# Optimization experiments

Hardware: AMD Instinct MI355X
Metric: run time of the kernel (lower is better)

The kernel has to match this reference:

```python
import jax, jax.numpy as jnp
import numpy as np
from jax import lax

NEG = -1000.0  # torch.full((N,S), -1000.0) init in dp_align


def setup_inputs() -> dict:
    key = jax.random.key(0)
    ks = jax.random.split(key, 4)
    N, S, h = 128, 2048, 256          # nodes, segments, hsize
    d = 2 * h                         # bi-LSTM output dim = 2*hsize
    seg_text_feats = jax.random.normal(ks[0], (N, d), jnp.float32)
    vid_feature = jax.random.normal(ks[1], (S, d), jnp.float32)
    # relation_query: Linear(4h, h) -> ReLU -> (Dropout, eval=identity) -> Linear(h, 1)
    W1 = jax.random.normal(ks[2], (h, 2 * d), jnp.float32) / np.sqrt(2.0 * d)
    b1 = jnp.zeros((h,), jnp.float32)
    W2 = jax.random.normal(ks[3], (1, h), jnp.float32) / np.sqrt(float(h))
    b2 = jnp.zeros((1,), jnp.float32)
    return {"seg_text_feats": seg_text_feats, "vid_feature": vid_feature,
            "W1": W1, "b1": b1, "W2": W2, "b2": b2}


def reference(seg_text_feats, vid_feature, W1, b1, W2, b2):
    N, d = seg_text_feats.shape
    S = vid_feature.shape[0]
    # Pairwise MLP logits for every (node, segment) cell, vectorized:
    # concat(text, vid) @ W1^T == text @ W1[:, :d]^T + vid @ W1[:, d:]^T
    A = seg_text_feats @ W1[:, :d].T           # [N, h]
    B = vid_feature @ W1[:, d:].T              # [S, h]
    H = jax.nn.relu(A[:, None, :] + B[None, :, :] + b1)   # [N, S, h]
    logits = jnp.einsum('nsh,h->ns', H, W2[0]) + b2[0]     # [N, S]
    logsig = jax.nn.log_sigmoid(logits)

    n_idx = jnp.arange(N)
    # DP over columns, right to left. prev_col is arr[:, s+1] (virtual col S = NEG).
    def step(prev_col, s):
        ls = logsig[:, s]
        nxt = jnp.concatenate([prev_col[1:], jnp.full((1,), NEG, prev_col.dtype)])  # arr[n+1, s+1]
        curr = ls + jnp.where(n_idx == N - 1, 0.0, nxt)   # last node: no chain term
        take = curr >= prev_col                            # tie -> take current (matches >=)
        val = jnp.where(take, curr, prev_col)
        in_range = (s >= n_idx) & (s <= S - N + n_idx)     # start_ind/end_ind bands
        col = jnp.where(in_range, val, NEG)
        return col, take

    _, takes = lax.scan(step, jnp.full((N,), NEG), jnp.arange(S - 1, -1, -1))
    take_curr = takes[::-1].T                              # [N, S]

    # Backtrack parent pointers from (node 0, segment 0).
    def walk(carry, s):
        n, align = carry
        nc = jnp.minimum(n, N - 1)
        tc = take_curr[nc, s] & (n < N)
        align = align.at[nc].set(jnp.where(tc, s, align[nc]))
        return (n + tc.astype(jnp.int32), align), None

    (_, align), _ = lax.scan(walk, (jnp.int32(0), jnp.zeros((N,), jnp.int32)), jnp.arange(S))

    aggregated_logits = jnp.mean(logits[n_idx, align])     # sum(logit)/num_nodes
    adj_matrix = jnp.zeros((N + S, N + S), jnp.float32).at[S + n_idx, align].set(1.0)
    return adj_matrix, aggregated_logits
```

## Files before the change

kernel.cpp:

```cpp
#include <hip/hip_runtime.h>
#include <math.h>

#define NEGC (-1000.0f)

__global__ __launch_bounds__(256) void k1z_gemm(
    const float* __restrict__ seg, const float* __restrict__ vid,
    const float* __restrict__ W1, const float* __restrict__ b1,
    float* __restrict__ A2, float* __restrict__ B2, float4* __restrict__ out4)
{
    if (blockIdx.x >= 136) {
        const int i = (blockIdx.x - 136) * 256 + threadIdx.x;
        if (i < 1183744) out4[i] = make_float4(0.f, 0.f, 0.f, 0.f);
        return;
    }
    __shared__ float Xs[32][64];
    __shared__ float Ws[32][64];
    const int tid = threadIdx.x;
    const int tx = tid & 15, ty = tid >> 4;
    const int lr = tid >> 2;
    const int lk = (tid & 3) * 8;
    const int colBase = (blockIdx.x & 3) * 64;
    const int rowBase = (blockIdx.x >> 2) * 64;
    const bool isSeg = (rowBase < 128);
    const float* __restrict__ X = isSeg ? seg : vid;
    const int xRow = isSeg ? rowBase : (rowBase - 128);
    const int wOff = isSeg ? 0 : 512;

    float acc[4][4] = {};

    for (int k0 = 0; k0 < 512; k0 += 32) {
        const float* xp = X + (size_t)(xRow + lr) * 512 + (k0 + lk);
        const float4 xa = *(const float4*)xp;
        const float4 xb = *(const float4*)(xp + 4);
        const float* wp = W1 + (size_t)(colBase + lr) * 1024 + (wOff + k0 + lk);
        const float4 wa = *(const float4*)wp;
        const float4 wb = *(const float4*)(wp + 4);
        __syncthreads();
        Xs[lk + 0][lr] = xa.x; Xs[lk + 1][lr] = xa.y;
        Xs[lk + 2][lr] = xa.z; Xs[lk + 3][lr] = xa.w;
        Xs[lk + 4][lr] = xb.x; Xs[lk + 5][lr] = xb.y;
        Xs[lk + 6][lr] = xb.z; Xs[lk + 7][lr] = xb.w;
        Ws[lk + 0][lr] = wa.x; Ws[lk + 1][lr] = wa.y;
        Ws[lk + 2][lr] = wa.z; Ws[lk + 3][lr] = wa.w;
        Ws[lk + 4][lr] = wb.x; Ws[lk + 5][lr] = wb.y;
        Ws[lk + 6][lr] = wb.z; Ws[lk + 7][lr] = wb.w;
        __syncthreads();
        #pragma unroll
        for (int kk = 0; kk < 32; ++kk) {
            const float4 a4 = *(const float4*)&Xs[kk][4 * ty];
            const float4 b4 = *(const float4*)&Ws[kk][4 * tx];
            const float* a = (const float*)&a4;
            const float* b = (const float*)&b4;
            #pragma unroll
            for (int i = 0; i < 4; ++i)
                #pragma unroll
                for (int j = 0; j < 4; ++j)
                    acc[i][j] = fmaf(a[i], b[j], acc[i][j]);
        }
    }

    float* __restrict__ outp = (isSeg ? A2 : B2) + (size_t)xRow * 256;
    const int c = colBase + 4 * tx;
    #pragma unroll
    for (int i = 0; i < 4; ++i) {
        float4 v = make_float4(acc[i][0], acc[i][1], acc[i][2], acc[i][3]);
        if (isSeg) {
            v.x += b1[c + 0]; v.y += b1[c + 1]; v.z += b1[c + 2]; v.w += b1[c + 3];
        }
        *(float4*)(outp + (size_t)(4 * ty + i) * 256 + c) = v;
    }
}

__global__ __launch_bounds__(256) void k2_logits(
    const float* __restrict__ A2, const float* __restrict__ B2,
    const float* __restrict__ W2, const float* __restrict__ b2p,
    float* __restrict__ logitsT, float* __restrict__ lsPK)
{
    __shared__ float As[32][64];
    __shared__ float Bs[32][64];
    __shared__ float w2s[256];
    const int tid = threadIdx.x;
    const int tx = tid & 15, ty = tid >> 4;
    const int lr = tid >> 2;
    const int lk = (tid & 3) * 8;
    const int nBase = blockIdx.x * 64;
    const int sBase = blockIdx.y * 64;
    w2s[tid] = W2[tid];
    const float b2v = b2p[0];

    float acc[4][4] = {};

    for (int k0 = 0; k0 < 256; k0 += 32) {
        const float* ap = A2 + (size_t)(nBase + lr) * 256 + (k0 + lk);
        const float4 aa = *(const float4*)ap;
        const float4 ab = *(const float4*)(ap + 4);
        const float* bp = B2 + (size_t)(sBase + lr) * 256 + (k0 + lk);
        const float4 ba = *(const float4*)bp;
        const float4 bb = *(const float4*)(bp + 4);
        __syncthreads();
        As[lk + 0][lr] = aa.x; As[lk + 1][lr] = aa.y;
        As[lk + 2][lr] = aa.z; As[lk + 3][lr] = aa.w;
        As[lk + 4][lr] = ab.x; As[lk + 5][lr] = ab.y;
        As[lk + 6][lr] = ab.z; As[lk + 7][lr] = ab.w;
        Bs[lk + 0][lr] = ba.x; Bs[lk + 1][lr] = ba.y;
        Bs[lk + 2][lr] = ba.z; Bs[lk + 3][lr] = ba.w;
        Bs[lk + 4][lr] = bb.x; Bs[lk + 5][lr] = bb.y;
        Bs[lk + 6][lr] = bb.z; Bs[lk + 7][lr] = bb.w;
        __syncthreads();
        #pragma unroll
        for (int kk = 0; kk < 32; ++kk) {
            const float w = w2s[k0 + kk];
            const float4 a4 = *(const float4*)&As[kk][4 * ty];
            const float4 b4 = *(const float4*)&Bs[kk][4 * tx];
            const float* a = (const float*)&a4;
            const float* b = (const float*)&b4;
            #pragma unroll
            for (int i = 0; i < 4; ++i)
                #pragma unroll
                for (int j = 0; j < 4; ++j)
                    acc[i][j] = fmaf(fmaxf(a[i] + b[j], 0.0f), w, acc[i][j]);
        }
    }

    const int nb = nBase + 4 * ty;
    const int s0 = sBase + 4 * tx;
    float lsv[4][4];
    #pragma unroll
    for (int j = 0; j < 4; ++j) {
        const int s = s0 + j;
        float4 lg;
        float* lgp = (float*)&lg;
        #pragma unroll
        for (int i = 0; i < 4; ++i) {
            const float x = acc[i][j] + b2v;
            lgp[i] = x;
            lsv[j][i] = fminf(x, 0.0f) - log1pf(expf(-fabsf(x)));
        }
        *(float4*)&logitsT[(size_t)s * 128 + nb] = lg;
    }
    #pragma unroll
    for (int m = 0; m < 2; ++m) {
        const size_t base = (size_t)(s0 / 2 + m) * 256 + 2 * nb;
        #pragma unroll
        for (int q = 0; q < 2; ++q) {
            float4 v = make_float4(lsv[2 * m][2 * q],     lsv[2 * m + 1][2 * q],
                                   lsv[2 * m][2 * q + 1], lsv[2 * m + 1][2 * q + 1]);
            *(float4*)&lsPK[base + 4 * q] = v;
        }
    }
}

__global__ __launch_bounds__(64, 1) void k3_dp(
    const float* __restrict__ lsPK, const float* __restrict__ logitsT,
    float* __restrict__ out)
{
    __shared__ unsigned takeW[128 * 65];
    __shared__ int alignSh[128];
    const int lane = threadIdx.x;
    const int n0 = 2 * lane, n1 = n0 + 1;
    const float4* __restrict__ ls4 = (const float4*)lsPK;

    float p0 = NEGC, p1 = NEGC;
    unsigned u0 = 2047u - (unsigned)n0;
    unsigned u1 = u0 - 1u;
    unsigned w0 = 0u, w1 = 0u;

    auto core = [&](float lx, float ly, float nx) {
        float c0, c1;
        unsigned long long cc;
        asm volatile(
            "v_add_f32 %[c0], %[lx], %[p1]\n\t"
            "v_add_f32 %[c1], %[ly], %[nx]\n\t"
            "v_cmp_ge_f32 vcc, %[c0], %[p0]\n\t"
            "v_cmp_ge_f32 %[cc], %[c1], %[p1]\n\t"
            "v_addc_co_u32 %[w0], vcc, %[w0], %[w0], vcc\n\t"
            "v_addc_co_u32 %[w1], %[cc], %[w1], %[w1], %[cc]\n\t"
            "v_max_f32 %[p0], %[c0], %[p0]\n\t"
            "v_max_f32 %[p1], %[c1], %[p1]\n\t"
            : [p0]"+v"(p0), [p1]"+v"(p1), [w0]"+v"(w0), [w1]"+v"(w1),
              [c0]"=&v"(c0), [c1]"=&v"(c1), [cc]"=&s"(cc)
            : [lx]"v"(lx), [ly]"v"(ly), [nx]"v"(nx)
            : "vcc");
    };

    auto stepF = [&](float lx, float ly) {
        float nxt1 = __int_as_float(__builtin_amdgcn_update_dpp(
            0, __float_as_int(p0), 0x130 , 0xf, 0xf, true));
        core(lx, ly, nxt1);
    };
    auto stepM = [&](float lx, float ly) {
        float nxt1 = __int_as_float(__builtin_amdgcn_update_dpp(
            0, __float_as_int(p0), 0x130, 0xf, 0xf, true));
        core(lx, ly, nxt1);
        p0 = (u0 <= 1920u) ? p0 : NEGC;
        p1 = (u1 <= 1920u) ? p1 : NEGC;
        --u0; --u1;
    };

    float4 B0[4], B1[4], B2[4], B3[4], B4[4], B5[4], B6[4], B7[4];
#define LOADG(B, H) { _Pragma("unroll") \
    for (int j = 0; j < 4; ++j) B[j] = ls4[(size_t)((1023 - 4 * (H) - j) * 64 + lane)]; }
#define STEPS_F(B) { _Pragma("unroll") \
    for (int j = 0; j < 4; ++j) { stepF(B[j].y, B[j].w); stepF(B[j].x, B[j].z); } }
#define STEPS_M(B) { _Pragma("unroll") \
    for (int j = 0; j < 4; ++j) { stepM(B[j].y, B[j].w); stepM(B[j].x, B[j].z); } }
#define FLUSH { takeW[n0 * 65 + wIdx] = w0; takeW[n1 * 65 + wIdx] = w1; \
                w0 = 0u; w1 = 0u; --wIdx; }
#define BODY(SM) \
    SM(B0); if (h +  8 < 256) LOADG(B0, h +  8); \
    SM(B1); if (h +  9 < 256) LOADG(B1, h +  9); \
    SM(B2); if (h + 10 < 256) LOADG(B2, h + 10); \
    SM(B3); FLUSH; if (h + 11 < 256) LOADG(B3, h + 11); \
    SM(B4); if (h + 12 < 256) LOADG(B4, h + 12); \
    SM(B5); if (h + 13 < 256) LOADG(B5, h + 13); \
    SM(B6); if (h + 14 < 256) LOADG(B6, h + 14); \
    SM(B7); FLUSH; if (h + 15 < 256) LOADG(B7, h + 15);

    LOADG(B0, 0) LOADG(B1, 1) LOADG(B2, 2) LOADG(B3, 3)
    LOADG(B4, 4) LOADG(B5, 5) LOADG(B6, 6) LOADG(B7, 7)
    int wIdx = 63;
    for (int h = 0; h < 16; h += 8) { BODY(STEPS_M) }
    for (int h = 16; h < 240; h += 8) { BODY(STEPS_F) }
    u0 = (unsigned)(127 - n0);
    u1 = u0 - 1u;
    for (int h = 240; h < 256; h += 8) { BODY(STEPS_M) }
#undef BODY
#undef FLUSH
#undef STEPS_M
#undef STEPS_F
#undef LOADG

    alignSh[n0] = 0;
    alignSh[n1] = 0;
    __syncthreads();

    int pos = 0;
    for (int n = 0; n < 128; ++n) {
        unsigned w = takeW[n * 65 + lane];
        const int wi0 = pos >> 5;
        if (lane < wi0) w = 0u;
        else if (lane == wi0) w &= (0xFFFFFFFFu << (pos & 31));
        const unsigned long long m = __ballot(w != 0u);
        if (m == 0ull) break;
        const int fl = __builtin_ctzll(m);
        const unsigned fw = (unsigned)__builtin_amdgcn_readlane((int)w, fl);
        const int s = fl * 32 + __builtin_ctz(fw);
        if (lane == 0) alignSh[n] = s;
        pos = s + 1;
    }
    __syncthreads();

    const int a0 = alignSh[n0];
    const int a1 = alignSh[n1];
    out[(size_t)(2048 + n0) * 2176 + a0] = 1.0f;
    out[(size_t)(2048 + n1) * 2176 + a1] = 1.0f;
    float sum = logitsT[(size_t)a0 * 128 + n0] + logitsT[(size_t)a1 * 128 + n1];
    #pragma unroll
    for (int off = 32; off >= 1; off >>= 1) sum += __shfl_down(sum, off);
    if (lane == 0) out[(size_t)2176 * 2176] = sum * (1.0f / 128.0f);
}

extern "C" void kernel_launch(void* const* d_in, const int* in_sizes, int n_in,
                              void* d_out, int out_size, void* d_ws, size_t ws_size,
                              hipStream_t stream)
{
    const float* seg = (const float*)d_in[0];
    const float* vid = (const float*)d_in[1];
    const float* W1  = (const float*)d_in[2];
    const float* b1  = (const float*)d_in[3];
    const float* W2  = (const float*)d_in[4];
    const float* b2  = (const float*)d_in[5];
    float* out = (float*)d_out;
    float* ws  = (float*)d_ws;

    float* A2      = ws;
    float* B2      = ws + 32768;
    float* logitsT = ws + 557056;
    float* lsPK    = ws + 819200;

    k1z_gemm<<<dim3(4760), dim3(256), 0, stream>>>(seg, vid, W1, b1, A2, B2, (float4*)out);
    k2_logits<<<dim3(2, 32), dim3(256), 0, stream>>>(A2, B2, W2, b2, logitsT, lsPK);
    k3_dp<<<dim3(1), dim3(64), 0, stream>>>(lsPK, logitsT, out);
}
```

Measured before the change: 193.7 us.

## Use producer waves to stage DP inputs through double-buffered LDS ring

The serial DP kernel grows from one wave to four. Three producer waves prefetch log-sigmoid columns from global memory into a double-buffered shared-memory ring, while wave 0 consumes windows of 32 float4 columns from LDS. The aim is to take global-load latency off the single-wave critical path. In exchange it adds a block-wide barrier per window and LDS read latency on the consumer, and the backtrack now keeps alignments in registers instead of shared memory.

```diff
diff --git a/kernel.cpp b/kernel.cpp
--- a/kernel.cpp
+++ b/kernel.cpp
@@ -150,15 +150,33 @@
     }
 }
 
-__global__ __launch_bounds__(64, 1) void k3_dp(
+__global__ __launch_bounds__(256, 1) void k3_dp(
     const float* __restrict__ lsPK, const float* __restrict__ logitsT,
     float* __restrict__ out)
 {
+    __shared__ float4 ring[2][2048];
     __shared__ unsigned takeW[128 * 65];
-    __shared__ int alignSh[128];
-    const int lane = threadIdx.x;
+    const int tid = threadIdx.x;
+    const int wave = tid >> 6;
+    const int lane = tid & 63;
     const int n0 = 2 * lane, n1 = n0 + 1;
     const float4* __restrict__ ls4 = (const float4*)lsPK;
+
+    auto produce = [&](int k) {
+        const size_t base = (size_t)(992 - 32 * k) * 64 + lane;
+        const int p = wave - 1;
+        float4 t[11];
+        #pragma unroll
+        for (int i = 0; i < 11; ++i) {
+            const int c = p + 3 * i;
+            if (c < 32) t[i] = ls4[base + (size_t)c * 64];
+        }
+        #pragma unroll
+        for (int i = 0; i < 11; ++i) {
+            const int c = p + 3 * i;
+            if (c < 32) ring[k & 1][c * 64 + lane] = t[i];
+        }
+    };
 
     float p0 = NEGC, p1 = NEGC;
     unsigned u0 = 2047u - (unsigned)n0;
@@ -197,44 +215,52 @@
         --u0; --u1;
     };
 
-    float4 B0[4], B1[4], B2[4], B3[4], B4[4], B5[4], B6[4], B7[4];
-#define LOADG(B, H) { _Pragma("unroll") \
-    for (int j = 0; j < 4; ++j) B[j] = ls4[(size_t)((1023 - 4 * (H) - j) * 64 + lane)]; }
-#define STEPS_F(B) { _Pragma("unroll") \
-    for (int j = 0; j < 4; ++j) { stepF(B[j].y, B[j].w); stepF(B[j].x, B[j].z); } }
-#define STEPS_M(B) { _Pragma("unroll") \
-    for (int j = 0; j < 4; ++j) { stepM(B[j].y, B[j].w); stepM(B[j].x, B[j].z); } }
+    float4 C0, C1, C2, C3, N0, N1, N2, N3;
+    int wIdx = 63;
+#define RD(B, OFF) B = rb[(OFF) * 64 + lane];
+#define CONS4(STEP, Ba, Bb, Bc, Bd) { \
+    STEP(Ba.y, Ba.w); STEP(Ba.x, Ba.z); STEP(Bb.y, Bb.w); STEP(Bb.x, Bb.z); \
+    STEP(Bc.y, Bc.w); STEP(Bc.x, Bc.z); STEP(Bd.y, Bd.w); STEP(Bd.x, Bd.z); }
 #define FLUSH { takeW[n0 * 65 + wIdx] = w0; takeW[n1 * 65 + wIdx] = w1; \
                 w0 = 0u; w1 = 0u; --wIdx; }
-#define BODY(SM) \
-    SM(B0); if (h +  8 < 256) LOADG(B0, h +  8); \
-    SM(B1); if (h +  9 < 256) LOADG(B1, h +  9); \
-    SM(B2); if (h + 10 < 256) LOADG(B2, h + 10); \
-    SM(B3); FLUSH; if (h + 11 < 256) LOADG(B3, h + 11); \
-    SM(B4); if (h + 12 < 256) LOADG(B4, h + 12); \
-    SM(B5); if (h + 13 < 256) LOADG(B5, h + 13); \
-    SM(B6); if (h + 14 < 256) LOADG(B6, h + 14); \
-    SM(B7); FLUSH; if (h + 15 < 256) LOADG(B7, h + 15);
-
-    LOADG(B0, 0) LOADG(B1, 1) LOADG(B2, 2) LOADG(B3, 3)
-    LOADG(B4, 4) LOADG(B5, 5) LOADG(B6, 6) LOADG(B7, 7)
-    int wIdx = 63;
-    for (int h = 0; h < 16; h += 8) { BODY(STEPS_M) }
-    for (int h = 16; h < 240; h += 8) { BODY(STEPS_F) }
-    u0 = (unsigned)(127 - n0);
-    u1 = u0 - 1u;
-    for (int h = 240; h < 256; h += 8) { BODY(STEPS_M) }
-#undef BODY
+#define WINDOW(STEP) { \
+    RD(C0,31) RD(C1,30) RD(C2,29) RD(C3,28) \
+    RD(N0,27) RD(N1,26) RD(N2,25) RD(N3,24) CONS4(STEP,C0,C1,C2,C3) \
+    RD(C0,23) RD(C1,22) RD(C2,21) RD(C3,20) CONS4(STEP,N0,N1,N2,N3) \
+    RD(N0,19) RD(N1,18) RD(N2,17) RD(N3,16) CONS4(STEP,C0,C1,C2,C3) \
+    RD(C0,15) RD(C1,14) RD(C2,13) RD(C3,12) CONS4(STEP,N0,N1,N2,N3) FLUSH \
+    RD(N0,11) RD(N1,10) RD(N2, 9) RD(N3, 8) CONS4(STEP,C0,C1,C2,C3) \
+    RD(C0, 7) RD(C1, 6) RD(C2, 5) RD(C3, 4) CONS4(STEP,N0,N1,N2,N3) \
+    RD(N0, 3) RD(N1, 2) RD(N2, 1) RD(N3, 0) CONS4(STEP,C0,C1,C2,C3) \
+    CONS4(STEP,N0,N1,N2,N3) FLUSH }
+
+    if (wave > 0) produce(0);
+    __syncthreads();
+
+    for (int k = 0; k < 32; ++k) {
+        if (wave > 0) {
+            if (k + 1 < 32) produce(k + 1);
+        } else {
+            const float4* rb = &ring[k & 1][0];
+            if (k < 2) {
+                WINDOW(stepM)
+            } else if (k < 30) {
+                WINDOW(stepF)
+            } else {
+                if (k == 30) { u0 = (unsigned)(127 - n0); u1 = u0 - 1u; }
+                WINDOW(stepM)
+            }
+        }
+        __syncthreads();
+    }
+#undef WINDOW
 #undef FLUSH
-#undef STEPS_M
-#undef STEPS_F
-#undef LOADG
-
-    alignSh[n0] = 0;
-    alignSh[n1] = 0;
-    __syncthreads();
-
-    int pos = 0;
+#undef CONS4
+#undef RD
+
+    if (wave != 0) return;
+
+    int a0r = 0, a1r = 0, pos = 0;
     for (int n = 0; n < 128; ++n) {
         unsigned w = takeW[n * 65 + lane];
         const int wi0 = pos >> 5;
@@ -245,16 +271,14 @@
         const int fl = __builtin_ctzll(m);
         const unsigned fw = (unsigned)__builtin_amdgcn_readlane((int)w, fl);
         const int s = fl * 32 + __builtin_ctz(fw);
-        if (lane == 0) alignSh[n] = s;
+        if (n == n0) a0r = s;
+        if (n == n1) a1r = s;
         pos = s + 1;
     }
-    __syncthreads();
-
-    const int a0 = alignSh[n0];
-    const int a1 = alignSh[n1];
-    out[(size_t)(2048 + n0) * 2176 + a0] = 1.0f;
-    out[(size_t)(2048 + n1) * 2176 + a1] = 1.0f;
-    float sum = logitsT[(size_t)a0 * 128 + n0] + logitsT[(size_t)a1 * 128 + n1];
+
+    out[(size_t)(2048 + n0) * 2176 + a0r] = 1.0f;
+    out[(size_t)(2048 + n1) * 2176 + a1r] = 1.0f;
+    float sum = logitsT[(size_t)a0r * 128 + n0] + logitsT[(size_t)a1r * 128 + n1];
     #pragma unroll
     for (int off = 32; off >= 1; off >>= 1) sum += __shfl_down(sum, off);
     if (lane == 0) out[(size_t)2176 * 2176] = sum * (1.0f / 128.0f);
@@ -280,5 +304,5 @@
 
     k1z_gemm<<<dim3(4760), dim3(256), 0, stream>>>(seg, vid, W1, b1, A2, B2, (float4*)out);
     k2_logits<<<dim3(2, 32), dim3(256), 0, stream>>>(A2, B2, W2, b2, logitsT, lsPK);
-    k3_dp<<<dim3(1), dim3(64), 0, stream>>>(lsPK, logitsT, out);
+    k3_dp<<<dim3(1), dim3(256), 0, stream>>>(lsPK, logitsT, out);
 }
```

Measured after the change: 222.2 us. +14.7%, slower.

## Fuse GEMM, logits and DP kernels into one cooperative kernel with grid syncs

Applied to the files above, without the earlier changes.

Merges the three launches (projection GEMM plus output zeroing, pairwise logits, serial DP and backtrack) into a single cooperative kernel of 256 blocks separated by grid.sync barriers. Each block zeroes an equal slice of the output instead of using thousands of extra zero-fill blocks. The backtrack now keeps alignment indices in registers rather than shared memory. The aim is to remove inter-kernel launch gaps, at the cost of grid-barrier overhead, a larger shared-memory footprint per block, and heavier zeroing work per block.

```diff
diff --git a/kernel.cpp b/kernel.cpp
--- a/kernel.cpp
+++ b/kernel.cpp
@@ -1,203 +1,209 @@
 #include <hip/hip_runtime.h>
+#include <hip/hip_cooperative_groups.h>
 #include <math.h>
 
 #define NEGC (-1000.0f)
-
-__global__ __launch_bounds__(256) void k1z_gemm(
+namespace cg = cooperative_groups;
+
+__global__ __launch_bounds__(256, 1) void kfused(
     const float* __restrict__ seg, const float* __restrict__ vid,
     const float* __restrict__ W1, const float* __restrict__ b1,
-    float* __restrict__ A2, float* __restrict__ B2, float4* __restrict__ out4)
+    const float* __restrict__ W2, const float* __restrict__ b2p,
+    float* __restrict__ A2, float* __restrict__ B2,
+    float* __restrict__ logitsT, float* __restrict__ lsPK,
+    float* __restrict__ out)
 {
-    if (blockIdx.x >= 136) {
-        const int i = (blockIdx.x - 136) * 256 + threadIdx.x;
-        if (i < 1183744) out4[i] = make_float4(0.f, 0.f, 0.f, 0.f);
-        return;
-    }
     __shared__ float Xs[32][64];
     __shared__ float Ws[32][64];
+    __shared__ float w2s[256];
+    __shared__ unsigned takeW[128 * 65];
+
+    cg::grid_group grid = cg::this_grid();
+    const int bid = blockIdx.x;
     const int tid = threadIdx.x;
-    const int tx = tid & 15, ty = tid >> 4;
-    const int lr = tid >> 2;
-    const int lk = (tid & 3) * 8;
-    const int colBase = (blockIdx.x & 3) * 64;
-    const int rowBase = (blockIdx.x >> 2) * 64;
-    const bool isSeg = (rowBase < 128);
-    const float* __restrict__ X = isSeg ? seg : vid;
-    const int xRow = isSeg ? rowBase : (rowBase - 128);
-    const int wOff = isSeg ? 0 : 512;
-
-    float acc[4][4] = {};
-
-    for (int k0 = 0; k0 < 512; k0 += 32) {
-        const float* xp = X + (size_t)(xRow + lr) * 512 + (k0 + lk);
-        const float4 xa = *(const float4*)xp;
-        const float4 xb = *(const float4*)(xp + 4);
-        const float* wp = W1 + (size_t)(colBase + lr) * 1024 + (wOff + k0 + lk);
-        const float4 wa = *(const float4*)wp;
-        const float4 wb = *(const float4*)(wp + 4);
-        __syncthreads();
-        Xs[lk + 0][lr] = xa.x; Xs[lk + 1][lr] = xa.y;
-        Xs[lk + 2][lr] = xa.z; Xs[lk + 3][lr] = xa.w;
-        Xs[lk + 4][lr] = xb.x; Xs[lk + 5][lr] = xb.y;
-        Xs[lk + 6][lr] = xb.z; Xs[lk + 7][lr] = xb.w;
-        Ws[lk + 0][lr] = wa.x; Ws[lk + 1][lr] = wa.y;
-        Ws[lk + 2][lr] = wa.z; Ws[lk + 3][lr] = wa.w;
-        Ws[lk + 4][lr] = wb.x; Ws[lk + 5][lr] = wb.y;
-        Ws[lk + 6][lr] = wb.z; Ws[lk + 7][lr] = wb.w;
-        __syncthreads();
-        #pragma unroll
-        for (int kk = 0; kk < 32; ++kk) {
-            const float4 a4 = *(const float4*)&Xs[kk][4 * ty];
-            const float4 b4 = *(const float4*)&Ws[kk][4 * tx];
-            const float* a = (const float*)&a4;
-            const float* b = (const float*)&b4;
-            #pragma unroll
-            for (int i = 0; i < 4; ++i)
+
+    if (bid < 136) {
+        const int tx = tid & 15, ty = tid >> 4;
+        const int lr = tid >> 2;
+        const int lk = (tid & 3) * 8;
+        const int colBase = (bid & 3) * 64;
+        const int rowBase = (bid >> 2) * 64;
+        const bool isSeg = (rowBase < 128);
+        const float* __restrict__ X = isSeg ? seg : vid;
+        const int xRow = isSeg ? rowBase : (rowBase - 128);
+        const int wOff = isSeg ? 0 : 512;
+
+        float acc[4][4] = {};
+
+        for (int k0 = 0; k0 < 512; k0 += 32) {
+            const float* xp = X + (size_t)(xRow + lr) * 512 + (k0 + lk);
+            const float4 xa = *(const float4*)xp;
+            const float4 xb = *(const float4*)(xp + 4);
+            const float* wp = W1 + (size_t)(colBase + lr) * 1024 + (wOff + k0 + lk);
+            const float4 wa = *(const float4*)wp;
+            const float4 wb = *(const float4*)(wp + 4);
+            __syncthreads();
+            Xs[lk + 0][lr] = xa.x; Xs[lk + 1][lr] = xa.y;
+            Xs[lk + 2][lr] = xa.z; Xs[lk + 3][lr] = xa.w;
+            Xs[lk + 4][lr] = xb.x; Xs[lk + 5][lr] = xb.y;
+            Xs[lk + 6][lr] = xb.z; Xs[lk + 7][lr] = xb.w;
+            Ws[lk + 0][lr] = wa.x; Ws[lk + 1][lr] = wa.y;
+            Ws[lk + 2][lr] = wa.z; Ws[lk + 3][lr] = wa.w;
+            Ws[lk + 4][lr] = wb.x; Ws[lk + 5][lr] = wb.y;
+            Ws[lk + 6][lr] = wb.z; Ws[lk + 7][lr] = wb.w;
+            __syncthreads();
+            #pragma unroll
+            for (int kk = 0; kk < 32; ++kk) {
+                const float4 a4 = *(const float4*)&Xs[kk][4 * ty];
+                const float4 b4 = *(const float4*)&Ws[kk][4 * tx];
+                const float* a = (const float*)&a4;
+                const float* b = (const float*)&b4;
                 #pragma unroll
-                for (int j = 0; j < 4; ++j)
-                    acc[i][j] = fmaf(a[i], b[j], acc[i][j]);
-        }
-    }
-
-    float* __restrict__ outp = (isSeg ? A2 : B2) + (size_t)xRow * 256;
-    const int c = colBase + 4 * tx;
-    #pragma unroll
-    for (int i = 0; i < 4; ++i) {
-        float4 v = make_float4(acc[i][0], acc[i][1], acc[i][2], acc[i][3]);
-        if (isSeg) {
-            v.x += b1[c + 0]; v.y += b1[c + 1]; v.z += b1[c + 2]; v.w += b1[c + 3];
-        }
-        *(float4*)(outp + (size_t)(4 * ty + i) * 256 + c) = v;
-    }
-}
-
-__global__ __launch_bounds__(256) void k2_logits(
-    const float* __restrict__ A2, const float* __restrict__ B2,
-    const float* __restrict__ W2, const float* __restrict__ b2p,
-    float* __restrict__ logitsT, float* __restrict__ lsPK)
-{
-    __shared__ float As[32][64];
-    __shared__ float Bs[32][64];
-    __shared__ float w2s[256];
-    const int tid = threadIdx.x;
-    const int tx = tid & 15, ty = tid >> 4;
-    const int lr = tid >> 2;
-    const int lk = (tid & 3) * 8;
-    const int nBase = blockIdx.x * 64;
-    const int sBase = blockIdx.y * 64;
-    w2s[tid] = W2[tid];
-    const float b2v = b2p[0];
-
-    float acc[4][4] = {};
-
-    for (int k0 = 0; k0 < 256; k0 += 32) {
-        const float* ap = A2 + (size_t)(nBase + lr) * 256 + (k0 + lk);
-        const float4 aa = *(const float4*)ap;
-        const float4 ab = *(const float4*)(ap + 4);
-        const float* bp = B2 + (size_t)(sBase + lr) * 256 + (k0 + lk);
-        const float4 ba = *(const float4*)bp;
-        const float4 bb = *(const float4*)(bp + 4);
-        __syncthreads();
-        As[lk + 0][lr] = aa.x; As[lk + 1][lr] = aa.y;
-        As[lk + 2][lr] = aa.z; As[lk + 3][lr] = aa.w;
-        As[lk + 4][lr] = ab.x; As[lk + 5][lr] = ab.y;
-        As[lk + 6][lr] = ab.z; As[lk + 7][lr] = ab.w;
-        Bs[lk + 0][lr] = ba.x; Bs[lk + 1][lr] = ba.y;
-        Bs[lk + 2][lr] = ba.z; Bs[lk + 3][lr] = ba.w;
-        Bs[lk + 4][lr] = bb.x; Bs[lk + 5][lr] = bb.y;
-        Bs[lk + 6][lr] = bb.z; Bs[lk + 7][lr] = bb.w;
-        __syncthreads();
-        #pragma unroll
-        for (int kk = 0; kk < 32; ++kk) {
-            const float w = w2s[k0 + kk];
-            const float4 a4 = *(const float4*)&As[kk][4 * ty];
-            const float4 b4 = *(const float4*)&Bs[kk][4 * tx];
-            const float* a = (const float*)&a4;
-            const float* b = (const float*)&b4;
-            #pragma unroll
-            for (int i = 0; i < 4; ++i)
+                for (int i = 0; i < 4; ++i)
+                    #pragma unroll
+                    for (int j = 0; j < 4; ++j)
+                        acc[i][j] = fmaf(a[i], b[j], acc[i][j]);
+            }
+        }
+
+        float* __restrict__ outp = (isSeg ? A2 : B2) + (size_t)xRow * 256;
+        const int c = colBase + 4 * tx;
+        #pragma unroll
+        for (int i = 0; i < 4; ++i) {
+            float4 v = make_float4(acc[i][0], acc[i][1], acc[i][2], acc[i][3]);
+            if (isSeg) {
+                v.x += b1[c + 0]; v.y += b1[c + 1]; v.z += b1[c + 2]; v.w += b1[c + 3];
+            }
+            *(float4*)(outp + (size_t)(4 * ty + i) * 256 + c) = v;
+        }
+    }
+    {
+        float4* out4 = (float4*)out;
+        const int base = bid * 4624;
+        const float4 z = make_float4(0.f, 0.f, 0.f, 0.f);
+        for (int i = tid; i < 4624; i += 256) out4[base + i] = z;
+    }
+    grid.sync();
+
+    if (bid < 64) {
+        float (* __restrict__ As)[64] = Xs;
+        float (* __restrict__ Bs)[64] = Ws;
+        const int tx = tid & 15, ty = tid >> 4;
+        const int lr = tid >> 2;
+        const int lk = (tid & 3) * 8;
+        const int nBase = (bid & 1) * 64;
+        const int sBase = (bid >> 1) * 64;
+        w2s[tid] = W2[tid];
+        const float b2v = b2p[0];
+
+        float acc[4][4] = {};
+
+        for (int k0 = 0; k0 < 256; k0 += 32) {
+            const float* ap = A2 + (size_t)(nBase + lr) * 256 + (k0 + lk);
+            const float4 aa = *(const float4*)ap;
+            const float4 ab = *(const float4*)(ap + 4);
+            const float* bp = B2 + (size_t)(sBase + lr) * 256 + (k0 + lk);
+            const float4 ba = *(const float4*)bp;
+            const float4 bb = *(const float4*)(bp + 4);
+            __syncthreads();
+            As[lk + 0][lr] = aa.x; As[lk + 1][lr] = aa.y;
+            As[lk + 2][lr] = aa.z; As[lk + 3][lr] = aa.w;
+            As[lk + 4][lr] = ab.x; As[lk + 5][lr] = ab.y;
+            As[lk + 6][lr] = ab.z; As[lk + 7][lr] = ab.w;
+            Bs[lk + 0][lr] = ba.x; Bs[lk + 1][lr] = ba.y;
+            Bs[lk + 2][lr] = ba.z; Bs[lk + 3][lr] = ba.w;
+            Bs[lk + 4][lr] = bb.x; Bs[lk + 5][lr] = bb.y;
+            Bs[lk + 6][lr] = bb.z; Bs[lk + 7][lr] = bb.w;
+            __syncthreads();
+            #pragma unroll
+            for (int kk = 0; kk < 32; ++kk) {
+                const float w = w2s[k0 + kk];
+                const float4 a4 = *(const float4*)&As[kk][4 * ty];
+                const float4 b4 = *(const float4*)&Bs[kk][4 * tx];
+                const float* a = (const float*)&a4;
+                const float* b = (const float*)&b4;
                 #pragma unroll
-                for (int j = 0; j < 4; ++j)
-                    acc[i][j] = fmaf(fmaxf(a[i] + b[j], 0.0f), w, acc[i][j]);
-        }
-    }
-
-    const int nb = nBase + 4 * ty;
-    const int s0 = sBase + 4 * tx;
-    float lsv[4][4];
-    #pragma unroll
-    for (int j = 0; j < 4; ++j) {
-        const int s = s0 + j;
-        float4 lg;
-        float* lgp = (float*)&lg;
-        #pragma unroll
-        for (int i = 0; i < 4; ++i) {
-            const float x = acc[i][j] + b2v;
-            lgp[i] = x;
-            lsv[j][i] = fminf(x, 0.0f) - log1pf(expf(-fabsf(x)));
-        }
-        *(float4*)&logitsT[(size_t)s * 128 + nb] = lg;
-    }
-    #pragma unroll
-    for (int m = 0; m < 2; ++m) {
-        const size_t base = (size_t)(s0 / 2 + m) * 256 + 2 * nb;
-        #pragma unroll
-        for (int q = 0; q < 2; ++q) {
-            float4 v = make_float4(lsv[2 * m][2 * q],     lsv[2 * m + 1][2 * q],
-                                   lsv[2 * m][2 * q + 1], lsv[2 * m + 1][2 * q + 1]);
-            *(float4*)&lsPK[base + 4 * q] = v;
-        }
-    }
-}
-
-__global__ __launch_bounds__(64, 1) void k3_dp(
-    const float* __restrict__ lsPK, const float* __restrict__ logitsT,
-    float* __restrict__ out)
-{
-    __shared__ unsigned takeW[128 * 65];
-    __shared__ int alignSh[128];
-    const int lane = threadIdx.x;
-    const int n0 = 2 * lane, n1 = n0 + 1;
-    const float4* __restrict__ ls4 = (const float4*)lsPK;
-
-    float p0 = NEGC, p1 = NEGC;
-    unsigned u0 = 2047u - (unsigned)n0;
-    unsigned u1 = u0 - 1u;
-    unsigned w0 = 0u, w1 = 0u;
-
-    auto core = [&](float lx, float ly, float nx) {
-        float c0, c1;
-        unsigned long long cc;
-        asm volatile(
-            "v_add_f32 %[c0], %[lx], %[p1]\n\t"
-            "v_add_f32 %[c1], %[ly], %[nx]\n\t"
-            "v_cmp_ge_f32 vcc, %[c0], %[p0]\n\t"
-            "v_cmp_ge_f32 %[cc], %[c1], %[p1]\n\t"
-            "v_addc_co_u32 %[w0], vcc, %[w0], %[w0], vcc\n\t"
-            "v_addc_co_u32 %[w1], %[cc], %[w1], %[w1], %[cc]\n\t"
-            "v_max_f32 %[p0], %[c0], %[p0]\n\t"
-            "v_max_f32 %[p1], %[c1], %[p1]\n\t"
-            : [p0]"+v"(p0), [p1]"+v"(p1), [w0]"+v"(w0), [w1]"+v"(w1),
-              [c0]"=&v"(c0), [c1]"=&v"(c1), [cc]"=&s"(cc)
-            : [lx]"v"(lx), [ly]"v"(ly), [nx]"v"(nx)
-            : "vcc");
-    };
-
-    auto stepF = [&](float lx, float ly) {
-        float nxt1 = __int_as_float(__builtin_amdgcn_update_dpp(
-            0, __float_as_int(p0), 0x130 , 0xf, 0xf, true));
-        core(lx, ly, nxt1);
-    };
-    auto stepM = [&](float lx, float ly) {
-        float nxt1 = __int_as_float(__builtin_amdgcn_update_dpp(
-            0, __float_as_int(p0), 0x130, 0xf, 0xf, true));
-        core(lx, ly, nxt1);
-        p0 = (u0 <= 1920u) ? p0 : NEGC;
-        p1 = (u1 <= 1920u) ? p1 : NEGC;
-        --u0; --u1;
-    };
-
-    float4 B0[4], B1[4], B2[4], B3[4], B4[4], B5[4], B6[4], B7[4];
+                for (int i = 0; i < 4; ++i)
+                    #pragma unroll
+                    for (int j = 0; j < 4; ++j)
+                        acc[i][j] = fmaf(fmaxf(a[i] + b[j], 0.0f), w, acc[i][j]);
+            }
+        }
+
+        const int nb = nBase + 4 * ty;
+        const int s0 = sBase + 4 * tx;
+        float lsv[4][4];
+        #pragma unroll
+        for (int j = 0; j < 4; ++j) {
+            const int s = s0 + j;
+            float4 lg;
+            float* lgp = (float*)&lg;
+            #pragma unroll
+            for (int i = 0; i < 4; ++i) {
+                const float x = acc[i][j] + b2v;
+                lgp[i] = x;
+                lsv[j][i] = fminf(x, 0.0f) - log1pf(expf(-fabsf(x)));
+            }
+            *(float4*)&logitsT[(size_t)s * 128 + nb] = lg;
+        }
+        #pragma unroll
+        for (int m = 0; m < 2; ++m) {
+            const size_t base = (size_t)(s0 / 2 + m) * 256 + 2 * nb;
+            #pragma unroll
+            for (int q = 0; q < 2; ++q) {
+                float4 v = make_float4(lsv[2 * m][2 * q],     lsv[2 * m + 1][2 * q],
+                                       lsv[2 * m][2 * q + 1], lsv[2 * m + 1][2 * q + 1]);
+                *(float4*)&lsPK[base + 4 * q] = v;
+            }
+        }
+    }
+    grid.sync();
+
+    if (bid != 0 || tid >= 64) return;
+    {
+        const int lane = tid;
+        const int n0 = 2 * lane, n1 = n0 + 1;
+        const float4* __restrict__ ls4 = (const float4*)lsPK;
+
+        float p0 = NEGC, p1 = NEGC;
+        unsigned u0 = 2047u - (unsigned)n0;
+        unsigned u1 = u0 - 1u;
+        unsigned w0 = 0u, w1 = 0u;
+
+        auto core = [&](float lx, float ly, float nx) {
+            float c0, c1;
+            unsigned long long cc;
+            asm volatile(
+                "v_add_f32 %[c0], %[lx], %[p1]\n\t"
+                "v_add_f32 %[c1], %[ly], %[nx]\n\t"
+                "v_cmp_ge_f32 vcc, %[c0], %[p0]\n\t"
+                "v_cmp_ge_f32 %[cc], %[c1], %[p1]\n\t"
+                "v_addc_co_u32 %[w0], vcc, %[w0], %[w0], vcc\n\t"
+                "v_addc_co_u32 %[w1], %[cc], %[w1], %[w1], %[cc]\n\t"
+                "v_max_f32 %[p0], %[c0], %[p0]\n\t"
+                "v_max_f32 %[p1], %[c1], %[p1]\n\t"
+                : [p0]"+v"(p0), [p1]"+v"(p1), [w0]"+v"(w0), [w1]"+v"(w1),
+                  [c0]"=&v"(c0), [c1]"=&v"(c1), [cc]"=&s"(cc)
+                : [lx]"v"(lx), [ly]"v"(ly), [nx]"v"(nx)
+                : "vcc");
+        };
+
+        auto stepF = [&](float lx, float ly) {
+            float nxt1 = __int_as_float(__builtin_amdgcn_update_dpp(
+                0, __float_as_int(p0), 0x130 , 0xf, 0xf, true));
+            core(lx, ly, nxt1);
+        };
+        auto stepM = [&](float lx, float ly) {
+            float nxt1 = __int_as_float(__builtin_amdgcn_update_dpp(
+                0, __float_as_int(p0), 0x130, 0xf, 0xf, true));
+            core(lx, ly, nxt1);
+            p0 = (u0 <= 1920u) ? p0 : NEGC;
+            p1 = (u1 <= 1920u) ? p1 : NEGC;
+            --u0; --u1;
+        };
+
+        float4 B0[4], B1[4], B2r[4], B3[4], B4[4], B5[4], B6[4], B7[4];
+        int wIdx = 63;
 #define LOADG(B, H) { _Pragma("unroll") \
     for (int j = 0; j < 4; ++j) B[j] = ls4[(size_t)((1023 - 4 * (H) - j) * 64 + lane)]; }
 #define STEPS_F(B) { _Pragma("unroll") \
@@ -207,57 +213,51 @@
 #define FLUSH { takeW[n0 * 65 + wIdx] = w0; takeW[n1 * 65 + wIdx] = w1; \
                 w0 = 0u; w1 = 0u; --wIdx; }
 #define BODY(SM) \
-    SM(B0); if (h +  8 < 256) LOADG(B0, h +  8); \
-    SM(B1); if (h +  9 < 256) LOADG(B1, h +  9); \
-    SM(B2); if (h + 10 < 256) LOADG(B2, h + 10); \
-    SM(B3); FLUSH; if (h + 11 < 256) LOADG(B3, h + 11); \
-    SM(B4); if (h + 12 < 256) LOADG(B4, h + 12); \
-    SM(B5); if (h + 13 < 256) LOADG(B5, h + 13); \
-    SM(B6); if (h + 14 < 256) LOADG(B6, h + 14); \
-    SM(B7); FLUSH; if (h + 15 < 256) LOADG(B7, h + 15);
-
-    LOADG(B0, 0) LOADG(B1, 1) LOADG(B2, 2) LOADG(B3, 3)
-    LOADG(B4, 4) LOADG(B5, 5) LOADG(B6, 6) LOADG(B7, 7)
-    int wIdx = 63;
-    for (int h = 0; h < 16; h += 8) { BODY(STEPS_M) }
-    for (int h = 16; h < 240; h += 8) { BODY(STEPS_F) }
-    u0 = (unsigned)(127 - n0);
-    u1 = u0 - 1u;
-    for (int h = 240; h < 256; h += 8) { BODY(STEPS_M) }
+    SM(B0);  if (h +  8 < 256) LOADG(B0,  h +  8); \
+    SM(B1);  if (h +  9 < 256) LOADG(B1,  h +  9); \
+    SM(B2r); if (h + 10 < 256) LOADG(B2r, h + 10); \
+    SM(B3);  FLUSH; if (h + 11 < 256) LOADG(B3, h + 11); \
+    SM(B4);  if (h + 12 < 256) LOADG(B4,  h + 12); \
+    SM(B5);  if (h + 13 < 256) LOADG(B5,  h + 13); \
+    SM(B6);  if (h + 14 < 256) LOADG(B6,  h + 14); \
+    SM(B7);  FLUSH; if (h + 15 < 256) LOADG(B7, h + 15);
+
+        LOADG(B0, 0) LOADG(B1, 1) LOADG(B2r, 2) LOADG(B3, 3)
+        LOADG(B4, 4) LOADG(B5, 5) LOADG(B6, 6) LOADG(B7, 7)
+        for (int h = 0; h < 16; h += 8) { BODY(STEPS_M) }
+        for (int h = 16; h < 240; h += 8) { BODY(STEPS_F) }
+        u0 = (unsigned)(127 - n0);
+        u1 = u0 - 1u;
+        for (int h = 240; h < 256; h += 8) { BODY(STEPS_M) }
 #undef BODY
 #undef FLUSH
 #undef STEPS_M
 #undef STEPS_F
 #undef LOADG
 
-    alignSh[n0] = 0;
-    alignSh[n1] = 0;
-    __syncthreads();
-
-    int pos = 0;
-    for (int n = 0; n < 128; ++n) {
-        unsigned w = takeW[n * 65 + lane];
-        const int wi0 = pos >> 5;
-        if (lane < wi0) w = 0u;
-        else if (lane == wi0) w &= (0xFFFFFFFFu << (pos & 31));
-        const unsigned long long m = __ballot(w != 0u);
-        if (m == 0ull) break;
-        const int fl = __builtin_ctzll(m);
-        const unsigned fw = (unsigned)__builtin_amdgcn_readlane((int)w, fl);
-        const int s = fl * 32 + __builtin_ctz(fw);
-        if (lane == 0) alignSh[n] = s;
-        pos = s + 1;
-    }
-    __syncthreads();
-
-    const int a0 = alignSh[n0];
-    const int a1 = alignSh[n1];
-    out[(size_t)(2048 + n0) * 2176 + a0] = 1.0f;
-    out[(size_t)(2048 + n1) * 2176 + a1] = 1.0f;
-    float sum = logitsT[(size_t)a0 * 128 + n0] + logitsT[(size_t)a1 * 128 + n1];
-    #pragma unroll
-    for (int off = 32; off >= 1; off >>= 1) sum += __shfl_down(sum, off);
-    if (lane == 0) out[(size_t)2176 * 2176] = sum * (1.0f / 128.0f);
+        int a0r = 0, a1r = 0, pos = 0;
+        for (int n = 0; n < 128; ++n) {
+            unsigned w = takeW[n * 65 + lane];
+            const int wi0 = pos >> 5;
+            if (lane < wi0) w = 0u;
+            else if (lane == wi0) w &= (0xFFFFFFFFu << (pos & 31));
+            const unsigned long long m = __ballot(w != 0u);
+            if (m == 0ull) break;
+            const int fl = __builtin_ctzll(m);
+            const unsigned fw = (unsigned)__builtin_amdgcn_readlane((int)w, fl);
+            const int s = fl * 32 + __builtin_ctz(fw);
+            if (n == n0) a0r = s;
+            if (n == n1) a1r = s;
+            pos = s + 1;
+        }
+
+        out[(size_t)(2048 + n0) * 2176 + a0r] = 1.0f;
+        out[(size_t)(2048 + n1) * 2176 + a1r] = 1.0f;
+        float sum = logitsT[(size_t)a0r * 128 + n0] + logitsT[(size_t)a1r * 128 + n1];
+        #pragma unroll
+        for (int off = 32; off >= 1; off >>= 1) sum += __shfl_down(sum, off);
+        if (lane == 0) out[(size_t)2176 * 2176] = sum * (1.0f / 128.0f);
+    }
 }
 
 extern "C" void kernel_launch(void* const* d_in, const int* in_sizes, int n_in,
@@ -278,7 +278,10 @@
     float* logitsT = ws + 557056;
     float* lsPK    = ws + 819200;
 
-    k1z_gemm<<<dim3(4760), dim3(256), 0, stream>>>(seg, vid, W1, b1, A2, B2, (float4*)out);
-    k2_logits<<<dim3(2, 32), dim3(256), 0, stream>>>(A2, B2, W2, b2, logitsT, lsPK);
-    k3_dp<<<dim3(1), dim3(64), 0, stream>>>(lsPK, logitsT, out);
+    void* args[] = {
+        (void*)&seg, (void*)&vid, (void*)&W1, (void*)&b1, (void*)&W2, (void*)&b2,
+        (void*)&A2, (void*)&B2, (void*)&logitsT, (void*)&lsPK, (void*)&out
+    };
+    hipLaunchCooperativeKernel((const void*)kfused, dim3(256), dim3(256),
+                               args, 0, stream);
 }
```

New measurement: 267.9 us. +38.3%, slower.

## Fuse projection GEMM, output zeroing and logits kernels with a flag-based grid barrier

Applied to the files above, without the earlier changes.

Merges the first-layer projection GEMM, the zeroing of the adjacency output and the pairwise logits kernel into one 136-block launch. Blocks signal completion through per-block flags in workspace, block 0 gathers them and publishes a second flag, and the first 64 blocks then compute logits and log-sigmoid. This removes one kernel launch and the gap between launches. In exchange, output zeroing is spread over far fewer threads, and the magic-value flags are never reset, so on repeated calls the barrier may pass before the current call's A2/B2 writes have finished.

```diff
diff --git a/kernel.cpp b/kernel.cpp
--- a/kernel.cpp
+++ b/kernel.cpp
@@ -2,150 +2,175 @@
 #include <math.h>
 
 #define NEGC (-1000.0f)
-
-__global__ __launch_bounds__(256) void k1z_gemm(
+#define MAGICA 0x5137A9C1u
+#define MAGICB 0x2468ACE1u
+
+__global__ __launch_bounds__(256, 1) void kA(
     const float* __restrict__ seg, const float* __restrict__ vid,
     const float* __restrict__ W1, const float* __restrict__ b1,
-    float* __restrict__ A2, float* __restrict__ B2, float4* __restrict__ out4)
+    const float* __restrict__ W2, const float* __restrict__ b2p,
+    float* __restrict__ A2, float* __restrict__ B2,
+    float* __restrict__ logitsT, float* __restrict__ lsPK,
+    float* __restrict__ out, unsigned* __restrict__ flags)
 {
-    if (blockIdx.x >= 136) {
-        const int i = (blockIdx.x - 136) * 256 + threadIdx.x;
-        if (i < 1183744) out4[i] = make_float4(0.f, 0.f, 0.f, 0.f);
-        return;
-    }
     __shared__ float Xs[32][64];
     __shared__ float Ws[32][64];
+    __shared__ float w2s[256];
+    const int bid = blockIdx.x;
     const int tid = threadIdx.x;
     const int tx = tid & 15, ty = tid >> 4;
     const int lr = tid >> 2;
     const int lk = (tid & 3) * 8;
-    const int colBase = (blockIdx.x & 3) * 64;
-    const int rowBase = (blockIdx.x >> 2) * 64;
-    const bool isSeg = (rowBase < 128);
-    const float* __restrict__ X = isSeg ? seg : vid;
-    const int xRow = isSeg ? rowBase : (rowBase - 128);
-    const int wOff = isSeg ? 0 : 512;
-
-    float acc[4][4] = {};
-
-    for (int k0 = 0; k0 < 512; k0 += 32) {
-        const float* xp = X + (size_t)(xRow + lr) * 512 + (k0 + lk);
-        const float4 xa = *(const float4*)xp;
-        const float4 xb = *(const float4*)(xp + 4);
-        const float* wp = W1 + (size_t)(colBase + lr) * 1024 + (wOff + k0 + lk);
-        const float4 wa = *(const float4*)wp;
-        const float4 wb = *(const float4*)(wp + 4);
-        __syncthreads();
-        Xs[lk + 0][lr] = xa.x; Xs[lk + 1][lr] = xa.y;
-        Xs[lk + 2][lr] = xa.z; Xs[lk + 3][lr] = xa.w;
-        Xs[lk + 4][lr] = xb.x; Xs[lk + 5][lr] = xb.y;
-        Xs[lk + 6][lr] = xb.z; Xs[lk + 7][lr] = xb.w;
-        Ws[lk + 0][lr] = wa.x; Ws[lk + 1][lr] = wa.y;
-        Ws[lk + 2][lr] = wa.z; Ws[lk + 3][lr] = wa.w;
-        Ws[lk + 4][lr] = wb.x; Ws[lk + 5][lr] = wb.y;
-        Ws[lk + 6][lr] = wb.z; Ws[lk + 7][lr] = wb.w;
-        __syncthreads();
-        #pragma unroll
-        for (int kk = 0; kk < 32; ++kk) {
-            const float4 a4 = *(const float4*)&Xs[kk][4 * ty];
-            const float4 b4 = *(const float4*)&Ws[kk][4 * tx];
-            const float* a = (const float*)&a4;
-            const float* b = (const float*)&b4;
+
+    {
+        const int colBase = (bid & 3) * 64;
+        const int rowBase = (bid >> 2) * 64;
+        const bool isSeg = (rowBase < 128);
+        const float* __restrict__ X = isSeg ? seg : vid;
+        const int xRow = isSeg ? rowBase : (rowBase - 128);
+        const int wOff = isSeg ? 0 : 512;
+
+        float acc[4][4] = {};
+
+        for (int k0 = 0; k0 < 512; k0 += 32) {
+            const float* xp = X + (size_t)(xRow + lr) * 512 + (k0 + lk);
+            const float4 xa = *(const float4*)xp;
+            const float4 xb = *(const float4*)(xp + 4);
+            const float* wp = W1 + (size_t)(colBase + lr) * 1024 + (wOff + k0 + lk);
+            const float4 wa = *(const float4*)wp;
+            const float4 wb = *(const float4*)(wp + 4);
+            __syncthreads();
+            Xs[lk + 0][lr] = xa.x; Xs[lk + 1][lr] = xa.y;
+            Xs[lk + 2][lr] = xa.z; Xs[lk + 3][lr] = xa.w;
+            Xs[lk + 4][lr] = xb.x; Xs[lk + 5][lr] = xb.y;
+            Xs[lk + 6][lr] = xb.z; Xs[lk + 7][lr] = xb.w;
+            Ws[lk + 0][lr] = wa.x; Ws[lk + 1][lr] = wa.y;
+            Ws[lk + 2][lr] = wa.z; Ws[lk + 3][lr] = wa.w;
+            Ws[lk + 4][lr] = wb.x; Ws[lk + 5][lr] = wb.y;
+            Ws[lk + 6][lr] = wb.z; Ws[lk + 7][lr] = wb.w;
+            __syncthreads();
             #pragma unroll
-            for (int i = 0; i < 4; ++i)
+            for (int kk = 0; kk < 32; ++kk) {
+                const float4 a4 = *(const float4*)&Xs[kk][4 * ty];
+                const float4 b4 = *(const float4*)&Ws[kk][4 * tx];
+                const float* a = (const float*)&a4;
+                const float* b = (const float*)&b4;
                 #pragma unroll
-                for (int j = 0; j < 4; ++j)
-                    acc[i][j] = fmaf(a[i], b[j], acc[i][j]);
-        }
-    }
-
-    float* __restrict__ outp = (isSeg ? A2 : B2) + (size_t)xRow * 256;
-    const int c = colBase + 4 * tx;
-    #pragma unroll
-    for (int i = 0; i < 4; ++i) {
-        float4 v = make_float4(acc[i][0], acc[i][1], acc[i][2], acc[i][3]);
-        if (isSeg) {
-            v.x += b1[c + 0]; v.y += b1[c + 1]; v.z += b1[c + 2]; v.w += b1[c + 3];
-        }
-        *(float4*)(outp + (size_t)(4 * ty + i) * 256 + c) = v;
-    }
-}
-
-__global__ __launch_bounds__(256) void k2_logits(
-    const float* __restrict__ A2, const float* __restrict__ B2,
-    const float* __restrict__ W2, const float* __restrict__ b2p,
-    float* __restrict__ logitsT, float* __restrict__ lsPK)
-{
-    __shared__ float As[32][64];
-    __shared__ float Bs[32][64];
-    __shared__ float w2s[256];
-    const int tid = threadIdx.x;
-    const int tx = tid & 15, ty = tid >> 4;
-    const int lr = tid >> 2;
-    const int lk = (tid & 3) * 8;
-    const int nBase = blockIdx.x * 64;
-    const int sBase = blockIdx.y * 64;
-    w2s[tid] = W2[tid];
-    const float b2v = b2p[0];
-
-    float acc[4][4] = {};
-
-    for (int k0 = 0; k0 < 256; k0 += 32) {
-        const float* ap = A2 + (size_t)(nBase + lr) * 256 + (k0 + lk);
-        const float4 aa = *(const float4*)ap;
-        const float4 ab = *(const float4*)(ap + 4);
-        const float* bp = B2 + (size_t)(sBase + lr) * 256 + (k0 + lk);
-        const float4 ba = *(const float4*)bp;
-        const float4 bb = *(const float4*)(bp + 4);
-        __syncthreads();
-        As[lk + 0][lr] = aa.x; As[lk + 1][lr] = aa.y;
-        As[lk + 2][lr] = aa.z; As[lk + 3][lr] = aa.w;
-        As[lk + 4][lr] = ab.x; As[lk + 5][lr] = ab.y;
-        As[lk + 6][lr] = ab.z; As[lk + 7][lr] = ab.w;
-        Bs[lk + 0][lr] = ba.x; Bs[lk + 1][lr] = ba.y;
-        Bs[lk + 2][lr] = ba.z; Bs[lk + 3][lr] = ba.w;
-        Bs[lk + 4][lr] = bb.x; Bs[lk + 5][lr] = bb.y;
-        Bs[lk + 6][lr] = bb.z; Bs[lk + 7][lr] = bb.w;
-        __syncthreads();
-        #pragma unroll
-        for (int kk = 0; kk < 32; ++kk) {
-            const float w = w2s[k0 + kk];
-            const float4 a4 = *(const float4*)&As[kk][4 * ty];
-            const float4 b4 = *(const float4*)&Bs[kk][4 * tx];
-            const float* a = (const float*)&a4;
-            const float* b = (const float*)&b4;
-            #pragma unroll
-            for (int i = 0; i < 4; ++i)
-                #pragma unroll
-                for (int j = 0; j < 4; ++j)
-                    acc[i][j] = fmaf(fmaxf(a[i] + b[j], 0.0f), w, acc[i][j]);
-        }
-    }
-
-    const int nb = nBase + 4 * ty;
-    const int s0 = sBase + 4 * tx;
-    float lsv[4][4];
-    #pragma unroll
-    for (int j = 0; j < 4; ++j) {
-        const int s = s0 + j;
-        float4 lg;
-        float* lgp = (float*)&lg;
+                for (int i = 0; i < 4; ++i)
+                    #pragma unroll
+                    for (int j = 0; j < 4; ++j)
+                        acc[i][j] = fmaf(a[i], b[j], acc[i][j]);
+            }
+        }
+
+        float* __restrict__ outp = (isSeg ? A2 : B2) + (size_t)xRow * 256;
+        const int c = colBase + 4 * tx;
         #pragma unroll
         for (int i = 0; i < 4; ++i) {
-            const float x = acc[i][j] + b2v;
-            lgp[i] = x;
-            lsv[j][i] = fminf(x, 0.0f) - log1pf(expf(-fabsf(x)));
-        }
-        *(float4*)&logitsT[(size_t)s * 128 + nb] = lg;
-    }
-    #pragma unroll
-    for (int m = 0; m < 2; ++m) {
-        const size_t base = (size_t)(s0 / 2 + m) * 256 + 2 * nb;
+            float4 v = make_float4(acc[i][0], acc[i][1], acc[i][2], acc[i][3]);
+            if (isSeg) {
+                v.x += b1[c + 0]; v.y += b1[c + 1]; v.z += b1[c + 2]; v.w += b1[c + 3];
+            }
+            *(float4*)(outp + (size_t)(4 * ty + i) * 256 + c) = v;
+        }
+    }
+
+    {
+        float4* out4 = (float4*)out;
+        const float4 z = make_float4(0.f, 0.f, 0.f, 0.f);
+        const int base = bid * 8704 + tid;
         #pragma unroll
-        for (int q = 0; q < 2; ++q) {
-            float4 v = make_float4(lsv[2 * m][2 * q],     lsv[2 * m + 1][2 * q],
-                                   lsv[2 * m][2 * q + 1], lsv[2 * m + 1][2 * q + 1]);
-            *(float4*)&lsPK[base + 4 * q] = v;
+        for (int i = 0; i < 34; ++i) out4[base + i * 256] = z;
+    }
+
+    __syncthreads();
+    if (tid == 0)
+        __hip_atomic_store(&flags[bid], MAGICA, __ATOMIC_RELEASE, __HIP_MEMORY_SCOPE_AGENT);
+    if (bid == 0) {
+        if (tid < 136) {
+            while (__hip_atomic_load(&flags[tid], __ATOMIC_ACQUIRE,
+                                     __HIP_MEMORY_SCOPE_AGENT) != MAGICA)
+                __builtin_amdgcn_s_sleep(2);
+        }
+        __syncthreads();
+        if (tid == 0)
+            __hip_atomic_store(&flags[200], MAGICB, __ATOMIC_RELEASE, __HIP_MEMORY_SCOPE_AGENT);
+    }
+    if (bid >= 64) return;
+    if (tid == 0) {
+        while (__hip_atomic_load(&flags[200], __ATOMIC_ACQUIRE,
+                                 __HIP_MEMORY_SCOPE_AGENT) != MAGICB)
+            __builtin_amdgcn_s_sleep(2);
+    }
+    __syncthreads();
+
+    {
+        float (* __restrict__ As)[64] = Xs;
+        float (* __restrict__ Bs)[64] = Ws;
+        const int nBase = (bid & 1) * 64;
+        const int sBase = (bid >> 1) * 64;
+        w2s[tid] = W2[tid];
+        const float b2v = b2p[0];
+
+        float acc[4][4] = {};
+
+        for (int k0 = 0; k0 < 256; k0 += 32) {
+            const float* ap = A2 + (size_t)(nBase + lr) * 256 + (k0 + lk);
+            const float4 aa = *(const float4*)ap;
+            const float4 ab = *(const float4*)(ap + 4);
+            const float* bp = B2 + (size_t)(sBase + lr) * 256 + (k0 + lk);
+            const float4 ba = *(const float4*)bp;
+            const float4 bb = *(const float4*)(bp + 4);
+            __syncthreads();
+            As[lk + 0][lr] = aa.x; As[lk + 1][lr] = aa.y;
+            As[lk + 2][lr] = aa.z; As[lk + 3][lr] = aa.w;
+            As[lk + 4][lr] = ab.x; As[lk + 5][lr] = ab.y;
+            As[lk + 6][lr] = ab.z; As[lk + 7][lr] = ab.w;
+            Bs[lk + 0][lr] = ba.x; Bs[lk + 1][lr] = ba.y;
+            Bs[lk + 2][lr] = ba.z; Bs[lk + 3][lr] = ba.w;
+            Bs[lk + 4][lr] = bb.x; Bs[lk + 5][lr] = bb.y;
+            Bs[lk + 6][lr] = bb.z; Bs[lk + 7][lr] = bb.w;
+            __syncthreads();
+            #pragma unroll
+            for (int kk = 0; kk < 32; ++kk) {
+                const float w = w2s[k0 + kk];
+                const float4 a4 = *(const float4*)&As[kk][4 * ty];
+                const float4 b4 = *(const float4*)&Bs[kk][4 * tx];
+                const float* a = (const float*)&a4;
+                const float* b = (const float*)&b4;
+                #pragma unroll
+                for (int i = 0; i < 4; ++i)
+                    #pragma unroll
+                    for (int j = 0; j < 4; ++j)
+                        acc[i][j] = fmaf(fmaxf(a[i] + b[j], 0.0f), w, acc[i][j]);
+            }
+        }
+
+        const int nb = nBase + 4 * ty;
+        const int s0 = sBase + 4 * tx;
+        float lsv[4][4];
+        #pragma unroll
+        for (int j = 0; j < 4; ++j) {
+            const int s = s0 + j;
+            float4 lg;
+            float* lgp = (float*)&lg;
+            #pragma unroll
+            for (int i = 0; i < 4; ++i) {
+                const float x = acc[i][j] + b2v;
+                lgp[i] = x;
+                lsv[j][i] = fminf(x, 0.0f) - log1pf(expf(-fabsf(x)));
+            }
+            *(float4*)&logitsT[(size_t)s * 128 + nb] = lg;
+        }
+        #pragma unroll
+        for (int m = 0; m < 2; ++m) {
+            const size_t base = (size_t)(s0 / 2 + m) * 256 + 2 * nb;
+            #pragma unroll
+            for (int q = 0; q < 2; ++q) {
+                float4 v = make_float4(lsv[2 * m][2 * q],     lsv[2 * m + 1][2 * q],
+                                       lsv[2 * m][2 * q + 1], lsv[2 * m + 1][2 * q + 1]);
+                *(float4*)&lsPK[base + 4 * q] = v;
+            }
         }
     }
 }
@@ -277,8 +302,9 @@
     float* B2      = ws + 32768;
     float* logitsT = ws + 557056;
     float* lsPK    = ws + 819200;
-
-    k1z_gemm<<<dim3(4760), dim3(256), 0, stream>>>(seg, vid, W1, b1, A2, B2, (float4*)out);
-    k2_logits<<<dim3(2, 32), dim3(256), 0, stream>>>(A2, B2, W2, b2, logitsT, lsPK);
+    unsigned* flags = (unsigned*)(ws + 1081344);
+
+    kA<<<dim3(136), dim3(256), 0, stream>>>(seg, vid, W1, b1, W2, b2,
+                                            A2, B2, logitsT, lsPK, out, flags);
     k3_dp<<<dim3(1), dim3(64), 0, stream>>>(lsPK, logitsT, out);
 }
```

After: 200.0 us. 1.03x slower.
